# Performance work log

Measured on AMD Instinct MI355X. Metric: run time of the kernel, lower is better.

Reference implementation:

```python
import jax, jax.numpy as jnp
import numpy as np

N_SAMPLES = 64
N_AGENTS = 64          # agents per sample (fully connected subgraph)
N = N_SAMPLES * N_AGENTS
F_DIM = 128            # decoder_latent_size
EDIM = 2
ZDIM = 2 * F_DIM + EDIM
BN_EPS = 1e-5


def _build_edge_index():
    # fully-connected (no self loops) per sample, with node offsets, COO row-major
    idx = np.arange(N_AGENTS)
    rows = np.repeat(idx, N_AGENTS)
    cols = np.tile(idx, N_AGENTS)
    mask = rows != cols
    rows, cols = rows[mask], cols[mask]
    offs = (np.arange(N_SAMPLES) * N_AGENTS)[:, None]
    src = (rows[None, :] + offs).ravel().astype(np.int32)  # edge_index[0] = source j
    dst = (cols[None, :] + offs).ravel().astype(np.int32)  # edge_index[1] = target i
    return src, dst


def setup_inputs() -> dict:
    key = jax.random.key(0)
    ks = jax.random.split(key, 12)
    src, dst = _build_edge_index()
    s = 1.0 / np.sqrt(ZDIM)
    inp = {
        "gnn_in": jax.random.normal(ks[0], (N, F_DIM), dtype=jnp.float32),
        "centers": jax.random.normal(ks[1], (N, EDIM), dtype=jnp.float32),
        "src": jnp.asarray(src),
        "dst": jnp.asarray(dst),
        "Wf1": jax.random.normal(ks[2], (F_DIM, ZDIM), dtype=jnp.float32) * s,
        "bf1": jnp.zeros((F_DIM,), jnp.float32),
        "Ws1": jax.random.normal(ks[3], (F_DIM, ZDIM), dtype=jnp.float32) * s,
        "bs1": jnp.zeros((F_DIM,), jnp.float32),
        "g1": jnp.ones((F_DIM,), jnp.float32),
        "be1": jnp.zeros((F_DIM,), jnp.float32),
        "Wf2": jax.random.normal(ks[4], (F_DIM, ZDIM), dtype=jnp.float32) * s,
        "bf2": jnp.zeros((F_DIM,), jnp.float32),
        "Ws2": jax.random.normal(ks[5], (F_DIM, ZDIM), dtype=jnp.float32) * s,
        "bs2": jnp.zeros((F_DIM,), jnp.float32),
        "g2": jnp.ones((F_DIM,), jnp.float32),
        "be2": jnp.zeros((F_DIM,), jnp.float32),
    }
    return inp


def _cgconv(x, edge_attr, src, dst, Wf, bf, Ws, bs, gamma, beta):
    # z_ij = [x_i, x_j, e_ij]  (i = target = dst, j = source = src)
    z = jnp.concatenate([x[dst], x[src], edge_attr], axis=-1)        # [E, 2F+2]
    msg = jax.nn.sigmoid(z @ Wf.T + bf) * jax.nn.softplus(z @ Ws.T + bs)  # [E, F]
    agg = jax.ops.segment_sum(msg, dst, num_segments=N)              # [N, F]
    # BatchNorm1d (training mode: batch stats, biased var), then residual
    mean = agg.mean(axis=0)
    var = agg.var(axis=0)
    agg = (agg - mean) * jax.lax.rsqrt(var + BN_EPS) * gamma + beta
    return agg + x


def reference(gnn_in, centers, src, dst,
              Wf1, bf1, Ws1, bs1, g1, be1,
              Wf2, bf2, Ws2, bs2, g2, be2):
    edge_attr = centers[dst] - centers[src]                           # data[cols] - data[rows]
    x = jax.nn.relu(_cgconv(gnn_in, edge_attr, src, dst, Wf1, bf1, Ws1, bs1, g1, be1))
    out = jax.nn.relu(_cgconv(x, edge_attr, src, dst, Wf2, bf2, Ws2, bs2, g2, be2))
    # original splits per sample; uniform sample size -> concatenation == out itself
    return out
```

## Files before the change

kernel.cpp:

```cpp
#include <hip/hip_runtime.h>

constexpr int NS = 64;
constexpr int NA = 64;
constexpr int NN = NS * NA;
constexpr int FD = 128;
constexpr int ZD = 2 * FD + 2;
constexpr int FS = 16;
constexpr int NB = NS * (FD / FS);
constexpr int NT = 512;
constexpr int XPAD = 132;
constexpr float BN_EPS = 1e-5f;
constexpr float L2E = 1.44269504088896f;
constexpr float LN2 = 0.69314718055995f;

__device__ __forceinline__ void stage_w(
    float4 (*wlds)[FS], const float* __restrict__ Wf, const float* __restrict__ Ws,
    int fq, int t0, int tstep)
{
    for (int i = t0; i < FD * FS; i += tstep) {
        int k = i >> 4, fr = i & (FS - 1);
        int row = (fq * FS + fr) * ZD;
        wlds[k][fr] = make_float4(Wf[row + k], Wf[row + FD + k],
                                  Ws[row + k], Ws[row + FD + k]);
    }
}

__device__ __forceinline__ void layer_body(
    const float (*xs)[XPAD], const float2* cs, float2 (*q)[FS],
    const float4 (*wlds)[FS],
    const float* __restrict__ Wf, const float* __restrict__ Ws,
    const float* __restrict__ bf, const float* __restrict__ bs,
    int tid, int s, int fq,
    float* __restrict__ agg, float* __restrict__ pS, float* __restrict__ pSS)
{
    const int fl = tid & (FS - 1);
    const int ig = tid >> 4;
    const int f  = fq * FS + fl;
    const int base = s * NA;

    float aPf0=0.f,aQf0=0.f,aPs0=0.f,aQs0=0.f;
    float aPf1=0.f,aQf1=0.f,aPs1=0.f,aQs1=0.f;
    #pragma unroll 4
    for (int k = 0; k < FD; ++k) {
        float4 w = wlds[k][fl];
        float x0 = xs[ig][k];
        float x1 = xs[ig + 32][k];
        aPf0 = fmaf(x0, w.x, aPf0); aQf0 = fmaf(x0, w.y, aQf0);
        aPs0 = fmaf(x0, w.z, aPs0); aQs0 = fmaf(x0, w.w, aQs0);
        aPf1 = fmaf(x1, w.x, aPf1); aQf1 = fmaf(x1, w.y, aQf1);
        aPs1 = fmaf(x1, w.z, aPs1); aQs1 = fmaf(x1, w.w, aQs1);
    }
    float we0 = Wf[f*ZD + 2*FD], we1 = Wf[f*ZD + 2*FD + 1];
    float ws0 = Ws[f*ZD + 2*FD], ws1 = Ws[f*ZD + 2*FD + 1];
    float bfv = bf[f], bsv = bs[f];
    float2 c0 = cs[ig], c1 = cs[ig + 32];
    float cf0 = c0.x*we0 + c0.y*we1, cg0 = c0.x*ws0 + c0.y*ws1;
    float cf1 = c1.x*we0 + c1.y*we1, cg1 = c1.x*ws0 + c1.y*ws1;
    float Pf0 = aPf0 + cf0 + bfv, Ps0 = aPs0 + cg0 + bsv;
    float Pf1 = aPf1 + cf1 + bfv, Ps1 = aPs1 + cg1 + bsv;
    float Qf0 = aQf0 - cf0,       Qs0 = aQs0 - cg0;
    float Qf1 = aQf1 - cf1,       Qs1 = aQs1 - cg1;
    float2 p0 = make_float2(__builtin_amdgcn_exp2f(-Pf0*L2E), __builtin_amdgcn_exp2f(Ps0*L2E));
    float2 p1 = make_float2(__builtin_amdgcn_exp2f(-Pf1*L2E), __builtin_amdgcn_exp2f(Ps1*L2E));
    q[ig][fl]    = make_float2(__builtin_amdgcn_exp2f(-Qf0*L2E), __builtin_amdgcn_exp2f(Qs0*L2E));
    q[ig+32][fl] = make_float2(__builtin_amdgcn_exp2f(-Qf1*L2E), __builtin_amdgcn_exp2f(Qs1*L2E));
    __syncthreads();

    float a0=0.f, a1=0.f, b0=0.f, b1=0.f;
    #pragma unroll 4
    for (int j = 0; j < NA; j += 2) {
        float2 qa = q[j][fl];
        float2 qb = q[j+1][fl];
        a0 = fmaf(__builtin_amdgcn_rcpf(1.0f + p0.x*qa.x),
                  __builtin_amdgcn_logf(1.0f + p0.y*qa.y), a0);
        b0 = fmaf(__builtin_amdgcn_rcpf(1.0f + p1.x*qa.x),
                  __builtin_amdgcn_logf(1.0f + p1.y*qa.y), b0);
        a1 = fmaf(__builtin_amdgcn_rcpf(1.0f + p0.x*qb.x),
                  __builtin_amdgcn_logf(1.0f + p0.y*qb.y), a1);
        b1 = fmaf(__builtin_amdgcn_rcpf(1.0f + p1.x*qb.x),
                  __builtin_amdgcn_logf(1.0f + p1.y*qb.y), b1);
    }
    float aA = a0 + a1, aB = b0 + b1;
    {
        float2 qv0 = q[ig][fl];
        aA -= __builtin_amdgcn_rcpf(1.0f + p0.x*qv0.x) *
              __builtin_amdgcn_logf(1.0f + p0.y*qv0.y);
        float2 qv1 = q[ig+32][fl];
        aB -= __builtin_amdgcn_rcpf(1.0f + p1.x*qv1.x) *
              __builtin_amdgcn_logf(1.0f + p1.y*qv1.y);
    }
    aA *= LN2; aB *= LN2;
    agg[(base + ig) * FD + f]      = aA;
    agg[(base + ig + 32) * FD + f] = aB;

    __syncthreads();
    float* sm = (float*)q;
    sm[tid]      = aA + aB;
    sm[NT + tid] = aA*aA + aB*aB;
    __syncthreads();
    if (tid < FS) {
        float sv = 0.f, qv = 0.f;
        #pragma unroll
        for (int r = 0; r < 32; ++r) {
            sv += sm[r * FS + tid];
            qv += sm[NT + r * FS + tid];
        }
        pS [s * FD + fq * FS + tid] = sv;
        pSS[s * FD + fq * FS + tid] = qv;
    }
}

__global__ __launch_bounds__(NT) void layer1_kernel(
    const float* __restrict__ X0, const float* __restrict__ C,
    const float* __restrict__ Wf, const float* __restrict__ Ws,
    const float* __restrict__ bf, const float* __restrict__ bs,
    float* __restrict__ agg, float* __restrict__ pS, float* __restrict__ pSS)
{
    __shared__ float xs[NA][XPAD];
    __shared__ float2 q[NA][FS];
    __shared__ float4 wlds[FD][FS];
    __shared__ float2 cs[NA];
    int tid = threadIdx.x, bid = blockIdx.x;
    int s = bid & (NS - 1), fq = bid >> 6;
    int base = s * NA;
    stage_w(wlds, Wf, Ws, fq, tid, NT);
    const float4* Xv = (const float4*)(X0 + base * FD);
    for (int idx = tid; idx < NA * FD / 4; idx += NT) {
        int n = idx >> 5, k4 = idx & 31;
        *(float4*)&xs[n][k4 * 4] = Xv[idx];
    }
    if (tid < NA) cs[tid] = ((const float2*)C)[base + tid];
    __syncthreads();
    layer_body(xs, cs, q, wlds, Wf, Ws, bf, bs, tid, s, fq, agg, pS, pSS);
}

__global__ __launch_bounds__(NT) void layer2_kernel(
    const float* __restrict__ X0, const float* __restrict__ agg1,
    const float* __restrict__ C,
    const float* __restrict__ pS1, const float* __restrict__ pSS1,
    const float* __restrict__ g1, const float* __restrict__ be1,
    const float* __restrict__ Wf, const float* __restrict__ Ws,
    const float* __restrict__ bf, const float* __restrict__ bs,
    float* __restrict__ x1, float* __restrict__ agg2,
    float* __restrict__ pS2, float* __restrict__ pSS2)
{
    __shared__ float xs[NA][XPAD];
    __shared__ float2 q[NA][FS];
    __shared__ float4 wlds[FD][FS];
    __shared__ float2 cs[NA];
    __shared__ float bnsc[FD], bnsh[FD];
    int tid = threadIdx.x, bid = blockIdx.x;
    int s = bid & (NS - 1), fq = bid >> 6;
    int base = s * NA;
    if (tid < FD) {
        float sv = 0.f, qv = 0.f;
        #pragma unroll
        for (int s2 = 0; s2 < NS; ++s2) {
            sv += pS1[s2 * FD + tid];
            qv += pSS1[s2 * FD + tid];
        }
        float m  = sv * (1.0f / NN);
        float v  = qv * (1.0f / NN) - m * m;
        float sc = g1[tid] * rsqrtf(v + BN_EPS);
        bnsc[tid] = sc;
        bnsh[tid] = be1[tid] - m * sc;
    } else {
        stage_w(wlds, Wf, Ws, fq, tid - FD, NT - FD);
        if (tid >= NT - NA) cs[tid - (NT - NA)] = ((const float2*)C)[base + tid - (NT - NA)];
    }
    __syncthreads();
    const float4* Xv  = (const float4*)(X0 + base * FD);
    const float4* Av  = (const float4*)(agg1 + base * FD);
    float4*       X1v = (float4*)(x1 + base * FD);
    for (int idx = tid; idx < NA * FD / 4; idx += NT) {
        int n = idx >> 5, k4 = (idx & 31) * 4;
        float4 x = Xv[idx], a = Av[idx];
        float4 r;
        r.x = fmaxf(fmaf(a.x, bnsc[k4 + 0], bnsh[k4 + 0]) + x.x, 0.0f);
        r.y = fmaxf(fmaf(a.y, bnsc[k4 + 1], bnsh[k4 + 1]) + x.y, 0.0f);
        r.z = fmaxf(fmaf(a.z, bnsc[k4 + 2], bnsh[k4 + 2]) + x.z, 0.0f);
        r.w = fmaxf(fmaf(a.w, bnsc[k4 + 3], bnsh[k4 + 3]) + x.w, 0.0f);
        *(float4*)&xs[n][k4] = r;
        X1v[idx] = r;
    }
    __syncthreads();
    layer_body(xs, cs, q, wlds, Wf, Ws, bf, bs, tid, s, fq, agg2, pS2, pSS2);
}

__global__ __launch_bounds__(NT) void out_kernel(
    const float4* __restrict__ x1, const float4* __restrict__ agg2,
    const float* __restrict__ pS2, const float* __restrict__ pSS2,
    const float* __restrict__ g2, const float* __restrict__ be2,
    float4* __restrict__ out)
{
    __shared__ float sc[FD], sh[FD];
    int tid = threadIdx.x;
    if (tid < FD) {
        float sv = 0.f, qv = 0.f;
        #pragma unroll
        for (int s2 = 0; s2 < NS; ++s2) {
            sv += pS2[s2 * FD + tid];
            qv += pSS2[s2 * FD + tid];
        }
        float m  = sv * (1.0f / NN);
        float v  = qv * (1.0f / NN) - m * m;
        float scl = g2[tid] * rsqrtf(v + BN_EPS);
        sc[tid] = scl;
        sh[tid] = be2[tid] - m * scl;
    }
    __syncthreads();
    int idx = blockIdx.x * NT + tid;
    int f0 = (idx & 31) * 4;
    float4 xv = x1[idx], av = agg2[idx];
    float4 r;
    r.x = fmaxf(fmaf(av.x, sc[f0 + 0], sh[f0 + 0]) + xv.x, 0.0f);
    r.y = fmaxf(fmaf(av.y, sc[f0 + 1], sh[f0 + 1]) + xv.y, 0.0f);
    r.z = fmaxf(fmaf(av.z, sc[f0 + 2], sh[f0 + 2]) + xv.z, 0.0f);
    r.w = fmaxf(fmaf(av.w, sc[f0 + 3], sh[f0 + 3]) + xv.w, 0.0f);
    out[idx] = r;
}

extern "C" void kernel_launch(void* const* d_in, const int* in_sizes, int n_in,
                              void* d_out, int out_size, void* d_ws, size_t ws_size,
                              hipStream_t stream) {
    const float* gnn_in  = (const float*)d_in[0];
    const float* centers = (const float*)d_in[1];
    const float* Wf1 = (const float*)d_in[4];
    const float* bf1 = (const float*)d_in[5];
    const float* Ws1 = (const float*)d_in[6];
    const float* bs1 = (const float*)d_in[7];
    const float* g1  = (const float*)d_in[8];
    const float* be1 = (const float*)d_in[9];
    const float* Wf2 = (const float*)d_in[10];
    const float* bf2 = (const float*)d_in[11];
    const float* Ws2 = (const float*)d_in[12];
    const float* bs2 = (const float*)d_in[13];
    const float* g2  = (const float*)d_in[14];
    const float* be2 = (const float*)d_in[15];

    char* ws = (char*)d_ws;
    float* agg1  = (float*)(ws);
    float* agg2  = (float*)(ws + (2 << 20));
    float* x1    = (float*)(ws + (4 << 20));
    float* p1S   = (float*)(ws + (6 << 20));
    float* p1SS  = (float*)(ws + (6 << 20) + (32 << 10));
    float* p2S   = (float*)(ws + (6 << 20) + (64 << 10));
    float* p2SS  = (float*)(ws + (6 << 20) + (96 << 10));

    layer1_kernel<<<NB, NT, 0, stream>>>(gnn_in, centers, Wf1, Ws1, bf1, bs1,
                                         agg1, p1S, p1SS);
    layer2_kernel<<<NB, NT, 0, stream>>>(gnn_in, agg1, centers, p1S, p1SS, g1, be1,
                                         Wf2, Ws2, bf2, bs2, x1, agg2, p2S, p2SS);
    out_kernel<<<NN * FD / 4 / NT, NT, 0, stream>>>(
        (const float4*)x1, (const float4*)agg2, p2S, p2SS, g2, be2, (float4*)d_out);
}
```

Baseline: 130.9 us.

## Read weights directly from global memory and parallelize BN stat reduction

Drops the LDS staging of the transposed weight tile. Each thread now reads its own feature's weight rows straight from global memory as float2 pairs, and reads x in float4 chunks from LDS. This removes the strided, uncoalesced staging loop and its LDS footprint, but every thread now does per-k global loads that depend on L1/L2 hits. Within a wavefront, the 16 feature lanes read different rows, so those loads are poorly coalesced. In layer2, the BN statistic reduction over samples is split across all 512 threads with a shared-memory combine, instead of using 128 threads serially.

```diff
diff --git a/kernel.cpp b/kernel.cpp
--- a/kernel.cpp
+++ b/kernel.cpp
@@ -13,21 +13,8 @@
 constexpr float L2E = 1.44269504088896f;
 constexpr float LN2 = 0.69314718055995f;
 
-__device__ __forceinline__ void stage_w(
-    float4 (*wlds)[FS], const float* __restrict__ Wf, const float* __restrict__ Ws,
-    int fq, int t0, int tstep)
-{
-    for (int i = t0; i < FD * FS; i += tstep) {
-        int k = i >> 4, fr = i & (FS - 1);
-        int row = (fq * FS + fr) * ZD;
-        wlds[k][fr] = make_float4(Wf[row + k], Wf[row + FD + k],
-                                  Ws[row + k], Ws[row + FD + k]);
-    }
-}
-
 __device__ __forceinline__ void layer_body(
     const float (*xs)[XPAD], const float2* cs, float2 (*q)[FS],
-    const float4 (*wlds)[FS],
     const float* __restrict__ Wf, const float* __restrict__ Ws,
     const float* __restrict__ bf, const float* __restrict__ bs,
     int tid, int s, int fq,
@@ -38,17 +25,39 @@
     const int f  = fq * FS + fl;
     const int base = s * NA;
 
+    const float2* WfR = (const float2*)(Wf + f * ZD);
+    const float2* WsR = (const float2*)(Ws + f * ZD);
+
     float aPf0=0.f,aQf0=0.f,aPs0=0.f,aQs0=0.f;
     float aPf1=0.f,aQf1=0.f,aPs1=0.f,aQs1=0.f;
     #pragma unroll 4
-    for (int k = 0; k < FD; ++k) {
-        float4 w = wlds[k][fl];
-        float x0 = xs[ig][k];
-        float x1 = xs[ig + 32][k];
-        aPf0 = fmaf(x0, w.x, aPf0); aQf0 = fmaf(x0, w.y, aQf0);
-        aPs0 = fmaf(x0, w.z, aPs0); aQs0 = fmaf(x0, w.w, aQs0);
-        aPf1 = fmaf(x1, w.x, aPf1); aQf1 = fmaf(x1, w.y, aQf1);
-        aPs1 = fmaf(x1, w.z, aPs1); aQs1 = fmaf(x1, w.w, aQs1);
+    for (int k = 0; k < FD; k += 4) {
+        int h = k >> 1;
+        float4 x0 = *(const float4*)&xs[ig][k];
+        float4 x1 = *(const float4*)&xs[ig + 32][k];
+        float2 fA = WfR[h],      fB = WfR[h + 1];
+        float2 fC = WfR[h + 64], fD = WfR[h + 65];
+        float2 sA = WsR[h],      sB = WsR[h + 1];
+        float2 sC = WsR[h + 64], sD = WsR[h + 65];
+        aPf0 = fmaf(x0.x, fA.x, aPf0); aQf0 = fmaf(x0.x, fC.x, aQf0);
+        aPs0 = fmaf(x0.x, sA.x, aPs0); aQs0 = fmaf(x0.x, sC.x, aQs0);
+        aPf1 = fmaf(x1.x, fA.x, aPf1); aQf1 = fmaf(x1.x, fC.x, aQf1);
+        aPs1 = fmaf(x1.x, sA.x, aPs1); aQs1 = fmaf(x1.x, sC.x, aQs1);
+
+        aPf0 = fmaf(x0.y, fA.y, aPf0); aQf0 = fmaf(x0.y, fC.y, aQf0);
+        aPs0 = fmaf(x0.y, sA.y, aPs0); aQs0 = fmaf(x0.y, sC.y, aQs0);
+        aPf1 = fmaf(x1.y, fA.y, aPf1); aQf1 = fmaf(x1.y, fC.y, aQf1);
+        aPs1 = fmaf(x1.y, sA.y, aPs1); aQs1 = fmaf(x1.y, sC.y, aQs1);
+
+        aPf0 = fmaf(x0.z, fB.x, aPf0); aQf0 = fmaf(x0.z, fD.x, aQf0);
+        aPs0 = fmaf(x0.z, sB.x, aPs0); aQs0 = fmaf(x0.z, sD.x, aQs0);
+        aPf1 = fmaf(x1.z, fB.x, aPf1); aQf1 = fmaf(x1.z, fD.x, aQf1);
+        aPs1 = fmaf(x1.z, sB.x, aPs1); aQs1 = fmaf(x1.z, sD.x, aQs1);
+
+        aPf0 = fmaf(x0.w, fB.y, aPf0); aQf0 = fmaf(x0.w, fD.y, aQf0);
+        aPs0 = fmaf(x0.w, sB.y, aPs0); aQs0 = fmaf(x0.w, sD.y, aQs0);
+        aPf1 = fmaf(x1.w, fB.y, aPf1); aQf1 = fmaf(x1.w, fD.y, aQf1);
+        aPs1 = fmaf(x1.w, sB.y, aPs1); aQs1 = fmaf(x1.w, sD.y, aQs1);
     }
     float we0 = Wf[f*ZD + 2*FD], we1 = Wf[f*ZD + 2*FD + 1];
     float ws0 = Ws[f*ZD + 2*FD], ws1 = Ws[f*ZD + 2*FD + 1];
@@ -116,14 +125,12 @@
     const float* __restrict__ bf, const float* __restrict__ bs,
     float* __restrict__ agg, float* __restrict__ pS, float* __restrict__ pSS)
 {
-    __shared__ float xs[NA][XPAD];
+    __shared__ __align__(16) float xs[NA][XPAD];
     __shared__ float2 q[NA][FS];
-    __shared__ float4 wlds[FD][FS];
     __shared__ float2 cs[NA];
     int tid = threadIdx.x, bid = blockIdx.x;
     int s = bid & (NS - 1), fq = bid >> 6;
     int base = s * NA;
-    stage_w(wlds, Wf, Ws, fq, tid, NT);
     const float4* Xv = (const float4*)(X0 + base * FD);
     for (int idx = tid; idx < NA * FD / 4; idx += NT) {
         int n = idx >> 5, k4 = idx & 31;
@@ -131,7 +138,7 @@
     }
     if (tid < NA) cs[tid] = ((const float2*)C)[base + tid];
     __syncthreads();
-    layer_body(xs, cs, q, wlds, Wf, Ws, bf, bs, tid, s, fq, agg, pS, pSS);
+    layer_body(xs, cs, q, Wf, Ws, bf, bs, tid, s, fq, agg, pS, pSS);
 }
 
 __global__ __launch_bounds__(NT) void layer2_kernel(
@@ -144,29 +151,37 @@
     float* __restrict__ x1, float* __restrict__ agg2,
     float* __restrict__ pS2, float* __restrict__ pSS2)
 {
-    __shared__ float xs[NA][XPAD];
+    __shared__ __align__(16) float xs[NA][XPAD];
     __shared__ float2 q[NA][FS];
-    __shared__ float4 wlds[FD][FS];
     __shared__ float2 cs[NA];
     __shared__ float bnsc[FD], bnsh[FD];
     int tid = threadIdx.x, bid = blockIdx.x;
     int s = bid & (NS - 1), fq = bid >> 6;
     int base = s * NA;
-    if (tid < FD) {
+    {
+        int fr = tid & (FD - 1), sq = tid >> 7;
         float sv = 0.f, qv = 0.f;
         #pragma unroll
-        for (int s2 = 0; s2 < NS; ++s2) {
-            sv += pS1[s2 * FD + tid];
-            qv += pSS1[s2 * FD + tid];
+        for (int s2 = 0; s2 < NS / 4; ++s2) {
+            int si = sq * (NS / 4) + s2;
+            sv += pS1[si * FD + fr];
+            qv += pSS1[si * FD + fr];
         }
+        float* sm = (float*)q;
+        sm[tid] = sv;
+        sm[NT + tid] = qv;
+    }
+    if (tid < NA) cs[tid] = ((const float2*)C)[base + tid];
+    __syncthreads();
+    if (tid < FD) {
+        const float* sm = (const float*)q;
+        float sv = sm[tid] + sm[FD + tid] + sm[2*FD + tid] + sm[3*FD + tid];
+        float qv = sm[NT + tid] + sm[NT + FD + tid] + sm[NT + 2*FD + tid] + sm[NT + 3*FD + tid];
         float m  = sv * (1.0f / NN);
         float v  = qv * (1.0f / NN) - m * m;
         float sc = g1[tid] * rsqrtf(v + BN_EPS);
         bnsc[tid] = sc;
         bnsh[tid] = be1[tid] - m * sc;
-    } else {
-        stage_w(wlds, Wf, Ws, fq, tid - FD, NT - FD);
-        if (tid >= NT - NA) cs[tid - (NT - NA)] = ((const float2*)C)[base + tid - (NT - NA)];
     }
     __syncthreads();
     const float4* Xv  = (const float4*)(X0 + base * FD);
@@ -184,7 +199,7 @@
         X1v[idx] = r;
     }
     __syncthreads();
-    layer_body(xs, cs, q, wlds, Wf, Ws, bf, bs, tid, s, fq, agg2, pS2, pSS2);
+    layer_body(xs, cs, q, Wf, Ws, bf, bs, tid, s, fq, agg2, pS2, pSS2);
 }
 
 __global__ __launch_bounds__(NT) void out_kernel(
```

Result: slower. 164.9 us (+26.0%).

## Halve block size and give each thread four nodes with float4 LDS loads

Applied to the files above, without the earlier changes.

Block size drops from 512 to 256 threads, so each thread now computes four target nodes instead of two. This raises register-level reuse of each weight float4 and lets the node features be read from LDS as float4 vectors. The BN-statistics reduction in layer2 and the output kernel is split across all threads in two halves instead of the first 128 threads only. Weight staging now uses every thread. The cost is higher register pressure per thread and fewer waves per block to hide latency.

```diff
diff --git a/kernel.cpp b/kernel.cpp
--- a/kernel.cpp
+++ b/kernel.cpp
@@ -7,7 +7,7 @@
 constexpr int ZD = 2 * FD + 2;
 constexpr int FS = 16;
 constexpr int NB = NS * (FD / FS);
-constexpr int NT = 512;
+constexpr int NT = 256;
 constexpr int XPAD = 132;
 constexpr float BN_EPS = 1e-5f;
 constexpr float L2E = 1.44269504088896f;
@@ -15,9 +15,9 @@
 
 __device__ __forceinline__ void stage_w(
     float4 (*wlds)[FS], const float* __restrict__ Wf, const float* __restrict__ Ws,
-    int fq, int t0, int tstep)
-{
-    for (int i = t0; i < FD * FS; i += tstep) {
+    int fq, int tid)
+{
+    for (int i = tid; i < FD * FS; i += NT) {
         int k = i >> 4, fr = i & (FS - 1);
         int row = (fq * FS + fr) * ZD;
         wlds[k][fr] = make_float4(Wf[row + k], Wf[row + FD + k],
@@ -38,76 +38,90 @@
     const int f  = fq * FS + fl;
     const int base = s * NA;
 
-    float aPf0=0.f,aQf0=0.f,aPs0=0.f,aQs0=0.f;
-    float aPf1=0.f,aQf1=0.f,aPs1=0.f,aQs1=0.f;
-    #pragma unroll 4
-    for (int k = 0; k < FD; ++k) {
-        float4 w = wlds[k][fl];
-        float x0 = xs[ig][k];
-        float x1 = xs[ig + 32][k];
-        aPf0 = fmaf(x0, w.x, aPf0); aQf0 = fmaf(x0, w.y, aQf0);
-        aPs0 = fmaf(x0, w.z, aPs0); aQs0 = fmaf(x0, w.w, aQs0);
-        aPf1 = fmaf(x1, w.x, aPf1); aQf1 = fmaf(x1, w.y, aQf1);
-        aPs1 = fmaf(x1, w.z, aPs1); aQs1 = fmaf(x1, w.w, aQs1);
+    float aPf[4] = {0,0,0,0}, aQf[4] = {0,0,0,0};
+    float aPs[4] = {0,0,0,0}, aQs[4] = {0,0,0,0};
+    #pragma unroll 2
+    for (int k = 0; k < FD; k += 4) {
+        float4 w0 = wlds[k + 0][fl];
+        float4 w1 = wlds[k + 1][fl];
+        float4 w2 = wlds[k + 2][fl];
+        float4 w3 = wlds[k + 3][fl];
+        #pragma unroll
+        for (int t = 0; t < 4; ++t) {
+            float4 x = *(const float4*)&xs[ig + 16 * t][k];
+            aPf[t] = fmaf(x.x, w0.x, aPf[t]); aQf[t] = fmaf(x.x, w0.y, aQf[t]);
+            aPs[t] = fmaf(x.x, w0.z, aPs[t]); aQs[t] = fmaf(x.x, w0.w, aQs[t]);
+            aPf[t] = fmaf(x.y, w1.x, aPf[t]); aQf[t] = fmaf(x.y, w1.y, aQf[t]);
+            aPs[t] = fmaf(x.y, w1.z, aPs[t]); aQs[t] = fmaf(x.y, w1.w, aQs[t]);
+            aPf[t] = fmaf(x.z, w2.x, aPf[t]); aQf[t] = fmaf(x.z, w2.y, aQf[t]);
+            aPs[t] = fmaf(x.z, w2.z, aPs[t]); aQs[t] = fmaf(x.z, w2.w, aQs[t]);
+            aPf[t] = fmaf(x.w, w3.x, aPf[t]); aQf[t] = fmaf(x.w, w3.y, aQf[t]);
+            aPs[t] = fmaf(x.w, w3.z, aPs[t]); aQs[t] = fmaf(x.w, w3.w, aQs[t]);
+        }
     }
     float we0 = Wf[f*ZD + 2*FD], we1 = Wf[f*ZD + 2*FD + 1];
     float ws0 = Ws[f*ZD + 2*FD], ws1 = Ws[f*ZD + 2*FD + 1];
     float bfv = bf[f], bsv = bs[f];
-    float2 c0 = cs[ig], c1 = cs[ig + 32];
-    float cf0 = c0.x*we0 + c0.y*we1, cg0 = c0.x*ws0 + c0.y*ws1;
-    float cf1 = c1.x*we0 + c1.y*we1, cg1 = c1.x*ws0 + c1.y*ws1;
-    float Pf0 = aPf0 + cf0 + bfv, Ps0 = aPs0 + cg0 + bsv;
-    float Pf1 = aPf1 + cf1 + bfv, Ps1 = aPs1 + cg1 + bsv;
-    float Qf0 = aQf0 - cf0,       Qs0 = aQs0 - cg0;
-    float Qf1 = aQf1 - cf1,       Qs1 = aQs1 - cg1;
-    float2 p0 = make_float2(__builtin_amdgcn_exp2f(-Pf0*L2E), __builtin_amdgcn_exp2f(Ps0*L2E));
-    float2 p1 = make_float2(__builtin_amdgcn_exp2f(-Pf1*L2E), __builtin_amdgcn_exp2f(Ps1*L2E));
-    q[ig][fl]    = make_float2(__builtin_amdgcn_exp2f(-Qf0*L2E), __builtin_amdgcn_exp2f(Qs0*L2E));
-    q[ig+32][fl] = make_float2(__builtin_amdgcn_exp2f(-Qf1*L2E), __builtin_amdgcn_exp2f(Qs1*L2E));
-    __syncthreads();
-
-    float a0=0.f, a1=0.f, b0=0.f, b1=0.f;
-    #pragma unroll 4
+    float2 p[4];
+    #pragma unroll
+    for (int t = 0; t < 4; ++t) {
+        int n = ig + 16 * t;
+        float2 c = cs[n];
+        float cf = c.x * we0 + c.y * we1;
+        float cg = c.x * ws0 + c.y * ws1;
+        float Pf = aPf[t] + cf + bfv, Ps = aPs[t] + cg + bsv;
+        float Qf = aQf[t] - cf,       Qs = aQs[t] - cg;
+        p[t] = make_float2(__builtin_amdgcn_exp2f(-Pf * L2E),
+                           __builtin_amdgcn_exp2f( Ps * L2E));
+        q[n][fl] = make_float2(__builtin_amdgcn_exp2f(-Qf * L2E),
+                               __builtin_amdgcn_exp2f( Qs * L2E));
+    }
+    __syncthreads();
+
+    float e0[4] = {0,0,0,0}, e1[4] = {0,0,0,0};
+    #pragma unroll 2
     for (int j = 0; j < NA; j += 2) {
         float2 qa = q[j][fl];
-        float2 qb = q[j+1][fl];
-        a0 = fmaf(__builtin_amdgcn_rcpf(1.0f + p0.x*qa.x),
-                  __builtin_amdgcn_logf(1.0f + p0.y*qa.y), a0);
-        b0 = fmaf(__builtin_amdgcn_rcpf(1.0f + p1.x*qa.x),
-                  __builtin_amdgcn_logf(1.0f + p1.y*qa.y), b0);
-        a1 = fmaf(__builtin_amdgcn_rcpf(1.0f + p0.x*qb.x),
-                  __builtin_amdgcn_logf(1.0f + p0.y*qb.y), a1);
-        b1 = fmaf(__builtin_amdgcn_rcpf(1.0f + p1.x*qb.x),
-                  __builtin_amdgcn_logf(1.0f + p1.y*qb.y), b1);
-    }
-    float aA = a0 + a1, aB = b0 + b1;
-    {
-        float2 qv0 = q[ig][fl];
-        aA -= __builtin_amdgcn_rcpf(1.0f + p0.x*qv0.x) *
-              __builtin_amdgcn_logf(1.0f + p0.y*qv0.y);
-        float2 qv1 = q[ig+32][fl];
-        aB -= __builtin_amdgcn_rcpf(1.0f + p1.x*qv1.x) *
-              __builtin_amdgcn_logf(1.0f + p1.y*qv1.y);
-    }
-    aA *= LN2; aB *= LN2;
-    agg[(base + ig) * FD + f]      = aA;
-    agg[(base + ig + 32) * FD + f] = aB;
+        float2 qb = q[j + 1][fl];
+        #pragma unroll
+        for (int t = 0; t < 4; ++t) {
+            e0[t] = fmaf(__builtin_amdgcn_rcpf(1.0f + p[t].x * qa.x),
+                         __builtin_amdgcn_logf(1.0f + p[t].y * qa.y), e0[t]);
+            e1[t] = fmaf(__builtin_amdgcn_rcpf(1.0f + p[t].x * qb.x),
+                         __builtin_amdgcn_logf(1.0f + p[t].y * qb.y), e1[t]);
+        }
+    }
+    float av[4];
+    float ssum = 0.f, qsum = 0.f;
+    #pragma unroll
+    for (int t = 0; t < 4; ++t) {
+        int n = ig + 16 * t;
+        float a = e0[t] + e1[t];
+        float2 qv = q[n][fl];
+        a -= __builtin_amdgcn_rcpf(1.0f + p[t].x * qv.x) *
+             __builtin_amdgcn_logf(1.0f + p[t].y * qv.y);
+        a *= LN2;
+        agg[(base + n) * FD + f] = a;
+        av[t] = a;
+        ssum += a; qsum += a * a;
+    }
 
     __syncthreads();
     float* sm = (float*)q;
-    sm[tid]      = aA + aB;
-    sm[NT + tid] = aA*aA + aB*aB;
+    sm[tid]      = ssum;
+    sm[NT + tid] = qsum;
     __syncthreads();
     if (tid < FS) {
         float sv = 0.f, qv = 0.f;
         #pragma unroll
-        for (int r = 0; r < 32; ++r) {
+        for (int r = 0; r < 16; ++r) {
             sv += sm[r * FS + tid];
             qv += sm[NT + r * FS + tid];
         }
         pS [s * FD + fq * FS + tid] = sv;
         pSS[s * FD + fq * FS + tid] = qv;
     }
+    (void)av;
 }
 
 __global__ __launch_bounds__(NT) void layer1_kernel(
@@ -116,14 +130,14 @@
     const float* __restrict__ bf, const float* __restrict__ bs,
     float* __restrict__ agg, float* __restrict__ pS, float* __restrict__ pSS)
 {
-    __shared__ float xs[NA][XPAD];
+    __shared__ __align__(16) float xs[NA][XPAD];
+    __shared__ float4 wlds[FD][FS];
     __shared__ float2 q[NA][FS];
-    __shared__ float4 wlds[FD][FS];
     __shared__ float2 cs[NA];
     int tid = threadIdx.x, bid = blockIdx.x;
     int s = bid & (NS - 1), fq = bid >> 6;
     int base = s * NA;
-    stage_w(wlds, Wf, Ws, fq, tid, NT);
+    stage_w(wlds, Wf, Ws, fq, tid);
     const float4* Xv = (const float4*)(X0 + base * FD);
     for (int idx = tid; idx < NA * FD / 4; idx += NT) {
         int n = idx >> 5, k4 = idx & 31;
@@ -144,29 +158,39 @@
     float* __restrict__ x1, float* __restrict__ agg2,
     float* __restrict__ pS2, float* __restrict__ pSS2)
 {
-    __shared__ float xs[NA][XPAD];
+    __shared__ __align__(16) float xs[NA][XPAD];
+    __shared__ float4 wlds[FD][FS];
     __shared__ float2 q[NA][FS];
-    __shared__ float4 wlds[FD][FS];
     __shared__ float2 cs[NA];
     __shared__ float bnsc[FD], bnsh[FD];
     int tid = threadIdx.x, bid = blockIdx.x;
     int s = bid & (NS - 1), fq = bid >> 6;
     int base = s * NA;
+    stage_w(wlds, Wf, Ws, fq, tid);
+    {
+        int fr = tid & (FD - 1), sq = tid >> 7;
+        float sv = 0.f, qv = 0.f;
+        #pragma unroll
+        for (int s2 = 0; s2 < NS / 2; ++s2) {
+            int si = sq * (NS / 2) + s2;
+            sv += pS1[si * FD + fr];
+            qv += pSS1[si * FD + fr];
+        }
+        float* sm = (float*)q;
+        sm[tid] = sv;
+        sm[2 * NT + tid] = qv;
+    }
+    if (tid < NA) cs[tid] = ((const float2*)C)[base + tid];
+    __syncthreads();
     if (tid < FD) {
-        float sv = 0.f, qv = 0.f;
-        #pragma unroll
-        for (int s2 = 0; s2 < NS; ++s2) {
-            sv += pS1[s2 * FD + tid];
-            qv += pSS1[s2 * FD + tid];
-        }
+        const float* sm = (const float*)q;
+        float sv = sm[tid] + sm[FD + tid];
+        float qv = sm[2 * NT + tid] + sm[2 * NT + FD + tid];
         float m  = sv * (1.0f / NN);
         float v  = qv * (1.0f / NN) - m * m;
         float sc = g1[tid] * rsqrtf(v + BN_EPS);
         bnsc[tid] = sc;
         bnsh[tid] = be1[tid] - m * sc;
-    } else {
-        stage_w(wlds, Wf, Ws, fq, tid - FD, NT - FD);
-        if (tid >= NT - NA) cs[tid - (NT - NA)] = ((const float2*)C)[base + tid - (NT - NA)];
     }
     __syncthreads();
     const float4* Xv  = (const float4*)(X0 + base * FD);
@@ -193,15 +217,25 @@
     const float* __restrict__ g2, const float* __restrict__ be2,
     float4* __restrict__ out)
 {
+    __shared__ float sm[4 * NT];
     __shared__ float sc[FD], sh[FD];
     int tid = threadIdx.x;
+    {
+        int fr = tid & (FD - 1), sq = tid >> 7;
+        float sv = 0.f, qv = 0.f;
+        #pragma unroll
+        for (int s2 = 0; s2 < NS / 2; ++s2) {
+            int si = sq * (NS / 2) + s2;
+            sv += pS2[si * FD + fr];
+            qv += pSS2[si * FD + fr];
+        }
+        sm[tid] = sv;
+        sm[2 * NT + tid] = qv;
+    }
+    __syncthreads();
     if (tid < FD) {
-        float sv = 0.f, qv = 0.f;
-        #pragma unroll
-        for (int s2 = 0; s2 < NS; ++s2) {
-            sv += pS2[s2 * FD + tid];
-            qv += pSS2[s2 * FD + tid];
-        }
+        float sv = sm[tid] + sm[FD + tid];
+        float qv = sm[2 * NT + tid] + sm[2 * NT + FD + tid];
         float m  = sv * (1.0f / NN);
         float v  = qv * (1.0f / NN) - m * m;
         float scl = g2[tid] * rsqrtf(v + BN_EPS);
```

Measured after the change: 134.5 us. 1.03x slower.
